# Kernel tuning notes

Hardware: AMD Instinct MI355X
Metric: run time of the kernel (lower is better)

Reference implementation:

```python
import jax, jax.numpy as jnp
import numpy as np
import math

B, N, H = 2, 2048, 256
NUM_HEADS, HEAD_DIM = 8, 32
WIN = 32            # window_size
WIN_LEN = 2 * WIN + 1


def setup_inputs() -> dict:
    key = jax.random.key(0)
    ks = jax.random.split(key, 12)
    s = 0.02
    return {
        "x": jax.random.normal(ks[0], (B, N, 4, H), dtype=jnp.float32),
        "Wq": jax.random.normal(ks[1], (H, H), dtype=jnp.float32) * s,
        "bq": jnp.zeros((H,), jnp.float32),
        "Wk": jax.random.normal(ks[2], (H, H), dtype=jnp.float32) * s,
        "bk": jnp.zeros((H,), jnp.float32),
        "Wv": jax.random.normal(ks[3], (H, H), dtype=jnp.float32) * s,
        "bv": jnp.zeros((H,), jnp.float32),
        "Wo": jax.random.normal(ks[4], (H, 3 * H), dtype=jnp.float32) * s,
        "bo": jnp.zeros((3 * H,), jnp.float32),
        "Wvec": jax.random.normal(ks[5], (H, 2 * H), dtype=jnp.float32) * s,
        "alpha_dot": jnp.float32(1.0),
        "alpha_norm": jnp.float32(1.0),
        "Wg": jax.random.normal(ks[6], (2 * H, H), dtype=jnp.float32) * s,
        "bg": jnp.zeros((H,), jnp.float32),
    }


def reference(x, Wq, bq, Wk, bk, Wv, bv, Wo, bo, Wvec, alpha_dot, alpha_norm, Wg, bg):
    h, d = NUM_HEADS, HEAD_DIM
    scale = 1.0 / math.sqrt(d)

    x_scalar = x[:, :, 0]          # (B,N,H)
    vec = x[:, :, 1:4]             # (B,N,3,H)

    q = (x_scalar @ Wq + bq).reshape(B, N, h, d).transpose(0, 2, 1, 3)  # (B,h,N,d)
    k = (x_scalar @ Wk + bk).reshape(B, N, h, d).transpose(0, 2, 1, 3)
    v = (x_scalar @ Wv + bv).reshape(B, N, h, d).transpose(0, 2, 1, 3)

    vec_proj = vec @ Wvec                                # (B,N,3,2H)
    vec1, vec2 = vec_proj[..., :H], vec_proj[..., H:]
    vec_dot = (vec1 * vec2).sum(axis=-2)                 # (B,N,H)
    vec_norm = jnp.linalg.norm(vec, axis=2)              # (B,N,H)

    # (B,N,3,h,d) -> (B,h,N,3*d)
    vec_flat = vec.reshape(B, N, 3, h, d).transpose(0, 3, 1, 2, 4).reshape(B, h, N, 3 * d)

    # sliding-window attention via padded gather (matches torch unfold semantics)
    BH = B * h
    q_l = q.reshape(BH, N, d)
    k_l = k.reshape(BH, N, d)
    v_l = v.reshape(BH, N, d)
    vec_l = vec_flat.reshape(BH, N, 3 * d)

    pad = ((0, 0), (WIN, WIN), (0, 0))
    k_p = jnp.pad(k_l, pad)
    v_p = jnp.pad(v_l, pad)
    vec_p = jnp.pad(vec_l, pad)

    idx = jnp.arange(N)[:, None] + jnp.arange(WIN_LEN)[None, :]  # (N,WIN_LEN)
    k_win = k_p[:, idx]        # (BH,N,WIN_LEN,d)
    v_win = v_p[:, idx]
    vec_win = vec_p[:, idx]    # (BH,N,WIN_LEN,3d)

    attn_scores = jnp.einsum('bid,biwd->biw', q_l, k_win) * scale
    attn_weights = jax.nn.softmax(attn_scores, axis=-1)  # (BH,N,WIN_LEN)

    x_agg = jnp.einsum('biw,biwd->bid', attn_weights, v_win).reshape(B, h, N, d)
    vec_aggr = jnp.einsum('biw,biwd->bid', attn_weights, vec_win).reshape(B, h, N, 3 * d)

    x_out = x_agg.transpose(0, 2, 1, 3).reshape(B, N, H)
    vec_aggr = vec_aggr.reshape(B, h, N, 3, d).transpose(0, 2, 3, 1, 4).reshape(B, N, 3, H)

    invariants = jnp.concatenate([alpha_dot * vec_dot, alpha_norm * vec_norm], axis=-1)
    gate = jax.nn.sigmoid(invariants @ Wg + bg)[:, :, None, :]   # (B,N,1,H)
    vec_combined = gate * vec_aggr + vec                          # gated add mixing

    o = x_out @ Wo + bo
    o1, o2, o3 = o[..., :H], o[..., H:2 * H], o[..., 2 * H:]
    x_updated = vec_dot * o1 + vec_norm * o2 + o3

    x_final = jnp.concatenate([x_updated[:, :, None], vec_combined], axis=2)  # (B,N,4,H)
    return x_final, attn_weights
```

## Files before the change

### kernel.cpp

```cpp
#include <hip/hip_runtime.h>
#include <math.h>

#define Bc 2
#define Nn 2048
#define Hh 256
#define NH 8
#define Dd 32
#define WIN 32
#define WL 65
#define BN (Bc * Nn)

typedef __attribute__((ext_vector_type(8))) short bf16x8;
typedef __attribute__((ext_vector_type(4))) float f32x4;

__device__ inline short f2bf(float f) {
    union { float f; unsigned u; } v; v.f = f;
    unsigned r = v.u + 0x7fffu + ((v.u >> 16) & 1u);
    return (short)(r >> 16);
}

__global__ __launch_bounds__(256) void castx_kernel(
    const float* __restrict__ x, const float* __restrict__ alpha_norm,
    short* __restrict__ xs_bf, short* __restrict__ vec_bf,
    float* __restrict__ vec_norm, short* __restrict__ inv_bf) {
    const int idx = blockIdx.x * 256 + threadIdx.x;
    const int bn = idx >> 8, ch = idx & 255;
    const size_t base = (size_t)bn * 1024 + ch;
    const float xs = x[base];
    const float v0 = x[base + 256], v1 = x[base + 512], v2 = x[base + 768];
    xs_bf[(size_t)bn * 256 + ch] = f2bf(xs);
    vec_bf[((size_t)0 * BN + bn) * 256 + ch] = f2bf(v0);
    vec_bf[((size_t)1 * BN + bn) * 256 + ch] = f2bf(v1);
    vec_bf[((size_t)2 * BN + bn) * 256 + ch] = f2bf(v2);
    const float nrm = sqrtf(v0 * v0 + v1 * v1 + v2 * v2);
    vec_norm[(size_t)bn * 256 + ch] = nrm;
    inv_bf[(size_t)bn * 512 + 256 + ch] = f2bf(alpha_norm[0] * nrm);
}

__global__ __launch_bounds__(256) void castw_kernel(
    const float* __restrict__ Wq, const float* __restrict__ Wk, const float* __restrict__ Wv,
    const float* __restrict__ Wvec, const float* __restrict__ Wg, const float* __restrict__ Wo,
    short* __restrict__ WqkvT, short* __restrict__ WvecT,
    short* __restrict__ WgT, short* __restrict__ WoT) {
    __shared__ float Ts[32][33];
    const int t = threadIdx.x;
    const int cc = t & 31, r0 = t >> 5;
    const int id = blockIdx.x;
    const float* W; int ldw; short* WT; int ldwt; int n0s, k0, n0d;
    if (id < 192) {
        const int tn = id >> 3, tk = id & 7, sel = tn >> 3;
        W = sel == 0 ? Wq : (sel == 1 ? Wk : Wv); ldw = 256;
        n0s = (tn & 7) * 32; k0 = tk * 32; WT = WqkvT; ldwt = 256; n0d = tn * 32;
    } else if (id < 320) {
        const int id2 = id - 192, tn = id2 >> 3, tk = id2 & 7;
        W = Wvec; ldw = 512; n0s = tn * 32; k0 = tk * 32; WT = WvecT; ldwt = 256; n0d = n0s;
    } else if (id < 448) {
        const int id3 = id - 320, tn = id3 >> 4, tk = id3 & 15;
        W = Wg; ldw = 256; n0s = tn * 32; k0 = tk * 32; WT = WgT; ldwt = 512; n0d = n0s;
    } else {
        const int id4 = id - 448, tn = id4 >> 3, tk = id4 & 7;
        W = Wo; ldw = 768; n0s = tn * 32; k0 = tk * 32; WT = WoT; ldwt = 256; n0d = n0s;
    }
#pragma unroll
    for (int p = 0; p < 4; ++p) {
        const int rr = r0 + p * 8;
        Ts[rr][cc] = W[(size_t)(k0 + rr) * ldw + n0s + cc];
    }
    __syncthreads();
#pragma unroll
    for (int p = 0; p < 4; ++p) {
        const int rr = r0 + p * 8;
        WT[(size_t)(n0d + rr) * ldwt + k0 + cc] = f2bf(Ts[cc][rr]);
    }
}

template<int NT>
__device__ inline void gemm_tiles(const short* __restrict__ A, const short* __restrict__ BT,
                                  int K, int row0, int col0,
                                  short* As, short* Bs, f32x4 acc[2][NT]) {
    const int t = threadIdx.x;
    const int lane = t & 63, wid = t >> 6;
    const int wm = wid & 1, wn = wid >> 1;
    const int quad = lane >> 4, lm = lane & 15;
#pragma unroll
    for (int mt = 0; mt < 2; ++mt)
#pragma unroll
        for (int nt = 0; nt < NT; ++nt) {
            f32x4 z = {0.f, 0.f, 0.f, 0.f};
            acc[mt][nt] = z;
        }
    for (int k0 = 0; k0 < K; k0 += 32) {
        {
            const int row = t >> 2, cg = t & 3;
            *(bf16x8*)&As[row * 40 + cg * 8] =
                *(const bf16x8*)&A[(size_t)(row0 + row) * K + k0 + cg * 8];
        }
#pragma unroll
        for (int p = 0; p < NT / 2; ++p) {
            const int idx = t + p * 256;
            const int col = idx >> 2, cg = idx & 3;
            *(bf16x8*)&Bs[col * 40 + cg * 8] =
                *(const bf16x8*)&BT[(size_t)(col0 + col) * K + k0 + cg * 8];
        }
        __syncthreads();
        bf16x8 af[2], bfr[NT];
#pragma unroll
        for (int mt = 0; mt < 2; ++mt)
            af[mt] = *(bf16x8*)&As[(wm * 32 + mt * 16 + lm) * 40 + quad * 8];
#pragma unroll
        for (int nt = 0; nt < NT; ++nt)
            bfr[nt] = *(bf16x8*)&Bs[(wn * NT * 16 + nt * 16 + lm) * 40 + quad * 8];
#pragma unroll
        for (int mt = 0; mt < 2; ++mt)
#pragma unroll
            for (int nt = 0; nt < NT; ++nt)
                acc[mt][nt] = __builtin_amdgcn_mfma_f32_16x16x32_bf16(
                    af[mt], bfr[nt], acc[mt][nt], 0, 0, 0);
        __syncthreads();
    }
}

__global__ __launch_bounds__(256) void gemm_qkv(
    const short* __restrict__ A, const short* __restrict__ BT,
    const float* __restrict__ bq, const float* __restrict__ bk, const float* __restrict__ bv,
    short* __restrict__ Qb, short* __restrict__ Kb, short* __restrict__ Vb) {
    __shared__ short As[64 * 40];
    __shared__ short Bs[128 * 40];
    f32x4 acc[2][4];
    const int row0 = blockIdx.x * 64, col0 = blockIdx.y * 128;
    gemm_tiles<4>(A, BT, 256, row0, col0, As, Bs, acc);
    const int lane = threadIdx.x & 63, wid = threadIdx.x >> 6;
    const int wm = wid & 1, wn = wid >> 1, quad = lane >> 4, lm = lane & 15;
    const int chunk = col0 >> 8;
    short* dst = chunk == 0 ? Qb : (chunk == 1 ? Kb : Vb);
    const float* bias = chunk == 0 ? bq : (chunk == 1 ? bk : bv);
#pragma unroll
    for (int mt = 0; mt < 2; ++mt)
#pragma unroll
        for (int nt = 0; nt < 4; ++nt) {
            const int col = col0 + wn * 64 + nt * 16 + lm;
            const int cm = col & 255;
            const float bb = bias[cm];
#pragma unroll
            for (int r = 0; r < 4; ++r) {
                const int row = row0 + wm * 32 + mt * 16 + quad * 4 + r;
                dst[(size_t)row * 256 + cm] = f2bf(acc[mt][nt][r] + bb);
            }
        }
}

__global__ __launch_bounds__(256) void gemm_vecdot(
    const short* __restrict__ A, const short* __restrict__ BT,
    const float* __restrict__ alpha_dot,
    float* __restrict__ vec_dot, short* __restrict__ inv_bf) {
    __shared__ short As[3][64 * 40];
    __shared__ short Bs[2][64 * 40];
    const int row0 = blockIdx.x * 64, ch0 = blockIdx.y * 64;
    const int t = threadIdx.x, lane = t & 63, wid = t >> 6;
    const int wm = wid & 1, wn = wid >> 1, quad = lane >> 4, lm = lane & 15;
    f32x4 acc[3][2][2][2];
#pragma unroll
    for (int p = 0; p < 3; ++p)
#pragma unroll
        for (int h = 0; h < 2; ++h)
#pragma unroll
            for (int mt = 0; mt < 2; ++mt)
#pragma unroll
                for (int nt = 0; nt < 2; ++nt) {
                    f32x4 z = {0.f, 0.f, 0.f, 0.f};
                    acc[p][h][mt][nt] = z;
                }
    for (int k0 = 0; k0 < 256; k0 += 32) {
        const int row = t >> 2, cg = t & 3;
#pragma unroll
        for (int p = 0; p < 3; ++p)
            *(bf16x8*)&As[p][row * 40 + cg * 8] =
                *(const bf16x8*)&A[((size_t)p * BN + row0 + row) * 256 + k0 + cg * 8];
#pragma unroll
        for (int h = 0; h < 2; ++h)
            *(bf16x8*)&Bs[h][row * 40 + cg * 8] =
                *(const bf16x8*)&BT[(size_t)(h * 256 + ch0 + row) * 256 + k0 + cg * 8];
        __syncthreads();
        bf16x8 af[3][2], bfr[2][2];
#pragma unroll
        for (int p = 0; p < 3; ++p)
#pragma unroll
            for (int mt = 0; mt < 2; ++mt)
                af[p][mt] = *(bf16x8*)&As[p][(wm * 32 + mt * 16 + lm) * 40 + quad * 8];
#pragma unroll
        for (int h = 0; h < 2; ++h)
#pragma unroll
            for (int nt = 0; nt < 2; ++nt)
                bfr[h][nt] = *(bf16x8*)&Bs[h][(wn * 32 + nt * 16 + lm) * 40 + quad * 8];
#pragma unroll
        for (int p = 0; p < 3; ++p)
#pragma unroll
            for (int h = 0; h < 2; ++h)
#pragma unroll
                for (int mt = 0; mt < 2; ++mt)
#pragma unroll
                    for (int nt = 0; nt < 2; ++nt)
                        acc[p][h][mt][nt] = __builtin_amdgcn_mfma_f32_16x16x32_bf16(
                            af[p][mt], bfr[h][nt], acc[p][h][mt][nt], 0, 0, 0);
        __syncthreads();
    }
    const float ad = alpha_dot[0];
#pragma unroll
    for (int mt = 0; mt < 2; ++mt)
#pragma unroll
        for (int nt = 0; nt < 2; ++nt) {
            const int col = ch0 + wn * 32 + nt * 16 + lm;
#pragma unroll
            for (int r = 0; r < 4; ++r) {
                const int row = row0 + wm * 32 + mt * 16 + quad * 4 + r;
                float dot = 0.f;
#pragma unroll
                for (int p = 0; p < 3; ++p)
                    dot = fmaf(acc[p][0][mt][nt][r], acc[p][1][mt][nt][r], dot);
                vec_dot[(size_t)row * 256 + col] = dot;
                inv_bf[(size_t)row * 512 + col] = f2bf(ad * dot);
            }
        }
}

__global__ __launch_bounds__(256) void gemm_gate(
    const short* __restrict__ A, const short* __restrict__ BT,
    const float* __restrict__ bg, float* __restrict__ gate) {
    __shared__ short As[64 * 40];
    __shared__ short Bs[64 * 40];
    f32x4 acc[2][2];
    const int row0 = blockIdx.x * 64, col0 = blockIdx.y * 64;
    gemm_tiles<2>(A, BT, 512, row0, col0, As, Bs, acc);
    const int lane = threadIdx.x & 63, wid = threadIdx.x >> 6;
    const int wm = wid & 1, wn = wid >> 1, quad = lane >> 4, lm = lane & 15;
#pragma unroll
    for (int mt = 0; mt < 2; ++mt)
#pragma unroll
        for (int nt = 0; nt < 2; ++nt) {
            const int col = col0 + wn * 32 + nt * 16 + lm;
            const float bb = bg[col];
#pragma unroll
            for (int r = 0; r < 4; ++r) {
                const int row = row0 + wm * 32 + mt * 16 + quad * 4 + r;
                const float z = acc[mt][nt][r] + bb;
                gate[(size_t)row * 256 + col] = 1.f / (1.f + __expf(-z));
            }
        }
}

__global__ __launch_bounds__(256) void attn_fused(
    const short* __restrict__ Qb, const short* __restrict__ Kb,
    const short* __restrict__ Vb, const short* __restrict__ vec_bf,
    const float* __restrict__ gate, const float* __restrict__ x,
    float* __restrict__ attnw, float* __restrict__ out, short* __restrict__ xout_bf) {
    const int bh = blockIdx.x >> 6, tile = blockIdx.x & 63;
    const int b = bh >> 3, hd = bh & 7;
    const int i0 = tile * 32;
    const int t = threadIdx.x, lane = t & 63, wid = t >> 6;
    const int wm = wid & 1, wn = wid >> 1, quad = lane >> 4, lm = lane & 15;

    __shared__ __align__(16) short Qs[32 * 40];
    __shared__ __align__(16) short Ks[96 * 40];
    __shared__ __align__(16) float Sc[32 * 100];
    __shared__ __align__(16) short Pb[32 * 104];
    __shared__ __align__(16) short St[128 * 112];

    for (int idx = t; idx < 32 * 104 / 2; idx += 256) ((int*)Pb)[idx] = 0;
    if (t < 128) {
        const int row = t >> 2, cg = t & 3;
        *(bf16x8*)&Qs[row * 40 + cg * 8] =
            *(const bf16x8*)&Qb[((size_t)(b * Nn + i0 + row)) * 256 + hd * 32 + cg * 8];
    }
#pragma unroll
    for (int kk = 0; kk < 2; ++kk) {
        const int idx = t + kk * 256;
        if (idx < 384) {
            const int row = idx >> 2, cg = idx & 3;
            const int j = i0 - WIN + row;
            bf16x8 kv = {0, 0, 0, 0, 0, 0, 0, 0};
            if (j >= 0 && j < Nn)
                kv = *(const bf16x8*)&Kb[((size_t)(b * Nn + j)) * 256 + hd * 32 + cg * 8];
            *(bf16x8*)&Ks[row * 40 + cg * 8] = kv;
        }
    }
    {
        const int chunk = t >> 4, j0 = t & 15;
#pragma unroll
        for (int it = 0; it < 6; ++it) {
            const int jr = j0 + it * 16;
            const int j = i0 - WIN + jr;
            bf16x8 val = {0, 0, 0, 0, 0, 0, 0, 0};
            if (j >= 0 && j < Nn) {
                if (chunk < 4)
                    val = *(const bf16x8*)&Vb[((size_t)(b * Nn + j)) * 256 + hd * 32 + chunk * 8];
                else {
                    const int vc = (chunk - 4) >> 2, d0 = ((chunk - 4) & 3) * 8;
                    val = *(const bf16x8*)&vec_bf[((size_t)vc * BN + b * Nn + j) * 256 + hd * 32 + d0];
                }
            }
#pragma unroll
            for (int u = 0; u < 8; ++u) St[(chunk * 8 + u) * 112 + jr] = val[u];
        }
    }
    __syncthreads();

    {
        const bf16x8 aq = *(bf16x8*)&Qs[(wm * 16 + lm) * 40 + quad * 8];
#pragma unroll
        for (int nt = 0; nt < 3; ++nt) {
            const bf16x8 bk = *(bf16x8*)&Ks[((wn * 3 + nt) * 16 + lm) * 40 + quad * 8];
            f32x4 c = {0.f, 0.f, 0.f, 0.f};
            c = __builtin_amdgcn_mfma_f32_16x16x32_bf16(aq, bk, c, 0, 0, 0);
#pragma unroll
            for (int r = 0; r < 4; ++r)
                Sc[(wm * 16 + quad * 4 + r) * 100 + (wn * 3 + nt) * 16 + lm] = c[r];
        }
    }
    __syncthreads();

    {
        const int i = t >> 3, sub = t & 7;
        float s[9];
#pragma unroll
        for (int k = 0; k < 9; ++k) {
            const int w = sub + 8 * k;
            s[k] = (w <= 64) ? Sc[i * 100 + i + w] * 0.17677669529663687f : -1e30f;
        }
        float m = s[0];
#pragma unroll
        for (int k = 1; k < 9; ++k) m = fmaxf(m, s[k]);
#pragma unroll
        for (int off = 1; off < 8; off <<= 1) m = fmaxf(m, __shfl_xor(m, off, 64));
        float sum = 0.f;
#pragma unroll
        for (int k = 0; k < 9; ++k) {
            const float e = (sub + 8 * k <= 64) ? __expf(s[k] - m) : 0.f;
            s[k] = e;
            sum += e;
        }
#pragma unroll
        for (int off = 1; off < 8; off <<= 1) sum += __shfl_xor(sum, off, 64);
        const float inv = 1.f / sum;
        float* dst = &attnw[((size_t)bh * Nn + (i0 + i)) * WL];
#pragma unroll
        for (int k = 0; k < 9; ++k) {
            const int w = sub + 8 * k;
            if (w <= 64) {
                const float pw = s[k] * inv;
                dst[w] = pw;
                Pb[i * 104 + i + w] = f2bf(pw);
            }
        }
    }
    __syncthreads();

    f32x4 acc[4];
#pragma unroll
    for (int nt = 0; nt < 4; ++nt) {
        f32x4 z = {0.f, 0.f, 0.f, 0.f};
        acc[nt] = z;
    }
#pragma unroll
    for (int ks = 0; ks < 3; ++ks) {
        const bf16x8 ap = *(bf16x8*)&Pb[(wm * 16 + lm) * 104 + ks * 32 + quad * 8];
#pragma unroll
        for (int nt = 0; nt < 4; ++nt) {
            const bf16x8 bs = *(bf16x8*)&St[(wn * 64 + nt * 16 + lm) * 112 + ks * 32 + quad * 8];
            acc[nt] = __builtin_amdgcn_mfma_f32_16x16x32_bf16(ap, bs, acc[nt], 0, 0, 0);
        }
    }
#pragma unroll
    for (int nt = 0; nt < 4; ++nt) {
        const int dim = wn * 64 + nt * 16 + lm;
#pragma unroll
        for (int r = 0; r < 4; ++r) {
            const int i = wm * 16 + quad * 4 + r;
            const size_t bn = (size_t)(b * Nn + i0 + i);
            if (dim < 32) {
                xout_bf[bn * 256 + hd * 32 + dim] = f2bf(acc[nt][r]);
            } else {
                const int dm = dim - 32, c = dm >> 5, dd = dm & 31;
                const int ch = hd * 32 + dd;
                const float g = gate[bn * 256 + ch];
                const size_t off = bn * 1024 + (1 + c) * 256 + ch;
                out[off] = fmaf(g, acc[nt][r], x[off]);
            }
        }
    }
}

__global__ __launch_bounds__(256) void gemm_outf(
    const short* __restrict__ A, const short* __restrict__ BT,
    const float* __restrict__ bo,
    const float* __restrict__ vec_dot, const float* __restrict__ vec_norm,
    float* __restrict__ out) {
    __shared__ short As[64 * 40];
    __shared__ short Bs[3][64 * 40];
    const int row0 = blockIdx.x * 64, ch0 = blockIdx.y * 64;
    const int t = threadIdx.x, lane = t & 63, wid = t >> 6;
    const int wm = wid & 1, wn = wid >> 1, quad = lane >> 4, lm = lane & 15;
    f32x4 acc[3][2][2];
#pragma unroll
    for (int p = 0; p < 3; ++p)
#pragma unroll
        for (int mt = 0; mt < 2; ++mt)
#pragma unroll
            for (int nt = 0; nt < 2; ++nt) {
                f32x4 z = {0.f, 0.f, 0.f, 0.f};
                acc[p][mt][nt] = z;
            }
    for (int k0 = 0; k0 < 256; k0 += 32) {
        const int row = t >> 2, cg = t & 3;
        *(bf16x8*)&As[row * 40 + cg * 8] =
            *(const bf16x8*)&A[(size_t)(row0 + row) * 256 + k0 + cg * 8];
#pragma unroll
        for (int p = 0; p < 3; ++p)
            *(bf16x8*)&Bs[p][row * 40 + cg * 8] =
                *(const bf16x8*)&BT[(size_t)(p * 256 + ch0 + row) * 256 + k0 + cg * 8];
        __syncthreads();
        bf16x8 af[2], bfr[3][2];
#pragma unroll
        for (int mt = 0; mt < 2; ++mt)
            af[mt] = *(bf16x8*)&As[(wm * 32 + mt * 16 + lm) * 40 + quad * 8];
#pragma unroll
        for (int p = 0; p < 3; ++p)
#pragma unroll
            for (int nt = 0; nt < 2; ++nt)
                bfr[p][nt] = *(bf16x8*)&Bs[p][(wn * 32 + nt * 16 + lm) * 40 + quad * 8];
#pragma unroll
        for (int p = 0; p < 3; ++p)
#pragma unroll
            for (int mt = 0; mt < 2; ++mt)
#pragma unroll
                for (int nt = 0; nt < 2; ++nt)
                    acc[p][mt][nt] = __builtin_amdgcn_mfma_f32_16x16x32_bf16(
                        af[mt], bfr[p][nt], acc[p][mt][nt], 0, 0, 0);
        __syncthreads();
    }
#pragma unroll
    for (int mt = 0; mt < 2; ++mt)
#pragma unroll
        for (int nt = 0; nt < 2; ++nt) {
            const int col = ch0 + wn * 32 + nt * 16 + lm;
            const float b1 = bo[col], b2 = bo[256 + col], b3 = bo[512 + col];
#pragma unroll
            for (int r = 0; r < 4; ++r) {
                const int row = row0 + wm * 32 + mt * 16 + quad * 4 + r;
                const float o1 = acc[0][mt][nt][r] + b1;
                const float o2 = acc[1][mt][nt][r] + b2;
                const float o3 = acc[2][mt][nt][r] + b3;
                const float vd = vec_dot[(size_t)row * 256 + col];
                const float vn = vec_norm[(size_t)row * 256 + col];
                out[(size_t)row * 1024 + col] = vd * o1 + vn * o2 + o3;
            }
        }
}

extern "C" void kernel_launch(void* const* d_in, const int* in_sizes, int n_in,
                              void* d_out, int out_size, void* d_ws, size_t ws_size,
                              hipStream_t stream) {
    const float* x  = (const float*)d_in[0];
    const float* Wq = (const float*)d_in[1];
    const float* bq = (const float*)d_in[2];
    const float* Wk = (const float*)d_in[3];
    const float* bk = (const float*)d_in[4];
    const float* Wv = (const float*)d_in[5];
    const float* bv = (const float*)d_in[6];
    const float* Wo = (const float*)d_in[7];
    const float* bo = (const float*)d_in[8];
    const float* Wvec = (const float*)d_in[9];
    const float* alpha_dot  = (const float*)d_in[10];
    const float* alpha_norm = (const float*)d_in[11];
    const float* Wg = (const float*)d_in[12];
    const float* bg = (const float*)d_in[13];

    float* ws = (float*)d_ws;
    float* vec_dot  = ws;
    float* vec_norm = ws + 1048576;
    float* gate     = ws + 2097152;
    short* sb = (short*)(ws + 3145728);
    short* xs_bf   = sb;
    short* vec_bf  = sb + 1048576;
    short* inv_bf  = sb + 4194304;
    short* xout_bf = sb + 6291456;
    short* Q_bf    = sb + 7340032;
    short* K_bf    = sb + 8388608;
    short* V_bf    = sb + 9437184;
    short* WqkvT   = sb + 10485760;
    short* WvecT   = sb + 10682368;
    short* WgT     = sb + 10813440;
    short* WoT     = sb + 10944512;

    float* out = (float*)d_out;
    float* attnw = out + (size_t)Bc * Nn * 4 * Hh;

    castx_kernel<<<4096, 256, 0, stream>>>(x, alpha_norm, xs_bf, vec_bf, vec_norm, inv_bf);
    castw_kernel<<<640, 256, 0, stream>>>(Wq, Wk, Wv, Wvec, Wg, Wo,
                                          WqkvT, WvecT, WgT, WoT);
    gemm_qkv<<<dim3(64, 6), 256, 0, stream>>>(xs_bf, WqkvT, bq, bk, bv, Q_bf, K_bf, V_bf);
    gemm_vecdot<<<dim3(64, 4), 256, 0, stream>>>(vec_bf, WvecT, alpha_dot, vec_dot, inv_bf);
    gemm_gate<<<dim3(64, 4), 256, 0, stream>>>(inv_bf, WgT, bg, gate);
    attn_fused<<<1024, 256, 0, stream>>>(Q_bf, K_bf, V_bf, vec_bf, gate, x,
                                         attnw, out, xout_bf);
    gemm_outf<<<dim3(64, 4), 256, 0, stream>>>(xout_bf, WoT, bo, vec_dot, vec_norm, out);
}
```

Before: 152.8 us.

## Merge cast kernels, register-prefetch GEMM tiles, fuse softmax into QK MFMA wave

Merges the x-cast and weight-transpose kernels into one launch. Adds register prefetch of the next K-slice in the shared GEMM helper, gemm_vecdot and gemm_outf, so global loads overlap with the MFMA work. gemm_vecdot uses 32-column tiles on a doubled grid for more blocks. In the attention kernel the score MFMAs and softmax run in registers on two waves, which removes the Sc shared buffer, one barrier and the St padding. The trade-offs are higher register pressure and two of four waves sitting idle during softmax.

```diff
diff --git a/kernel.cpp b/kernel.cpp
--- a/kernel.cpp
+++ b/kernel.cpp
@@ -19,33 +19,33 @@
     return (short)(r >> 16);
 }
 
-__global__ __launch_bounds__(256) void castx_kernel(
+__global__ __launch_bounds__(256) void castxw_kernel(
     const float* __restrict__ x, const float* __restrict__ alpha_norm,
-    short* __restrict__ xs_bf, short* __restrict__ vec_bf,
-    float* __restrict__ vec_norm, short* __restrict__ inv_bf) {
-    const int idx = blockIdx.x * 256 + threadIdx.x;
-    const int bn = idx >> 8, ch = idx & 255;
-    const size_t base = (size_t)bn * 1024 + ch;
-    const float xs = x[base];
-    const float v0 = x[base + 256], v1 = x[base + 512], v2 = x[base + 768];
-    xs_bf[(size_t)bn * 256 + ch] = f2bf(xs);
-    vec_bf[((size_t)0 * BN + bn) * 256 + ch] = f2bf(v0);
-    vec_bf[((size_t)1 * BN + bn) * 256 + ch] = f2bf(v1);
-    vec_bf[((size_t)2 * BN + bn) * 256 + ch] = f2bf(v2);
-    const float nrm = sqrtf(v0 * v0 + v1 * v1 + v2 * v2);
-    vec_norm[(size_t)bn * 256 + ch] = nrm;
-    inv_bf[(size_t)bn * 512 + 256 + ch] = f2bf(alpha_norm[0] * nrm);
-}
-
-__global__ __launch_bounds__(256) void castw_kernel(
     const float* __restrict__ Wq, const float* __restrict__ Wk, const float* __restrict__ Wv,
     const float* __restrict__ Wvec, const float* __restrict__ Wg, const float* __restrict__ Wo,
+    short* __restrict__ xs_bf, short* __restrict__ vec_bf,
+    float* __restrict__ vec_norm, short* __restrict__ inv_bf,
     short* __restrict__ WqkvT, short* __restrict__ WvecT,
     short* __restrict__ WgT, short* __restrict__ WoT) {
     __shared__ float Ts[32][33];
+    if (blockIdx.x < 4096) {
+        const int idx = blockIdx.x * 256 + threadIdx.x;
+        const int bn = idx >> 8, ch = idx & 255;
+        const size_t base = (size_t)bn * 1024 + ch;
+        const float xs = x[base];
+        const float v0 = x[base + 256], v1 = x[base + 512], v2 = x[base + 768];
+        xs_bf[(size_t)bn * 256 + ch] = f2bf(xs);
+        vec_bf[((size_t)0 * BN + bn) * 256 + ch] = f2bf(v0);
+        vec_bf[((size_t)1 * BN + bn) * 256 + ch] = f2bf(v1);
+        vec_bf[((size_t)2 * BN + bn) * 256 + ch] = f2bf(v2);
+        const float nrm = sqrtf(v0 * v0 + v1 * v1 + v2 * v2);
+        vec_norm[(size_t)bn * 256 + ch] = nrm;
+        inv_bf[(size_t)bn * 512 + 256 + ch] = f2bf(alpha_norm[0] * nrm);
+        return;
+    }
     const int t = threadIdx.x;
     const int cc = t & 31, r0 = t >> 5;
-    const int id = blockIdx.x;
+    const int id = blockIdx.x - 4096;
     const float* W; int ldw; short* WT; int ldwt; int n0s, k0, n0d;
     if (id < 192) {
         const int tn = id >> 3, tk = id & 7, sel = tn >> 3;
@@ -82,6 +82,7 @@
     const int lane = t & 63, wid = t >> 6;
     const int wm = wid & 1, wn = wid >> 1;
     const int quad = lane >> 4, lm = lane & 15;
+    const int srow = t >> 2, scg = (t & 3) * 8;
 #pragma unroll
     for (int mt = 0; mt < 2; ++mt)
 #pragma unroll
@@ -89,20 +90,29 @@
             f32x4 z = {0.f, 0.f, 0.f, 0.f};
             acc[mt][nt] = z;
         }
+    bf16x8 pa = *(const bf16x8*)&A[(size_t)(row0 + srow) * K + scg];
+    bf16x8 pb[NT / 2];
+#pragma unroll
+    for (int p = 0; p < NT / 2; ++p) {
+        const int idx = t + p * 256;
+        pb[p] = *(const bf16x8*)&BT[(size_t)(col0 + (idx >> 2)) * K + (idx & 3) * 8];
+    }
     for (int k0 = 0; k0 < K; k0 += 32) {
-        {
-            const int row = t >> 2, cg = t & 3;
-            *(bf16x8*)&As[row * 40 + cg * 8] =
-                *(const bf16x8*)&A[(size_t)(row0 + row) * K + k0 + cg * 8];
-        }
+        *(bf16x8*)&As[srow * 40 + scg] = pa;
 #pragma unroll
         for (int p = 0; p < NT / 2; ++p) {
             const int idx = t + p * 256;
-            const int col = idx >> 2, cg = idx & 3;
-            *(bf16x8*)&Bs[col * 40 + cg * 8] =
-                *(const bf16x8*)&BT[(size_t)(col0 + col) * K + k0 + cg * 8];
+            *(bf16x8*)&Bs[(idx >> 2) * 40 + (idx & 3) * 8] = pb[p];
         }
         __syncthreads();
+        if (k0 + 32 < K) {
+            pa = *(const bf16x8*)&A[(size_t)(row0 + srow) * K + k0 + 32 + scg];
+#pragma unroll
+            for (int p = 0; p < NT / 2; ++p) {
+                const int idx = t + p * 256;
+                pb[p] = *(const bf16x8*)&BT[(size_t)(col0 + (idx >> 2)) * K + k0 + 32 + (idx & 3) * 8];
+            }
+        }
         bf16x8 af[2], bfr[NT];
 #pragma unroll
         for (int mt = 0; mt < 2; ++mt)
@@ -154,34 +164,40 @@
     const float* __restrict__ alpha_dot,
     float* __restrict__ vec_dot, short* __restrict__ inv_bf) {
     __shared__ short As[3][64 * 40];
-    __shared__ short Bs[2][64 * 40];
-    const int row0 = blockIdx.x * 64, ch0 = blockIdx.y * 64;
+    __shared__ short Bs[2][32 * 40];
+    const int row0 = blockIdx.x * 64, ch0 = blockIdx.y * 32;
     const int t = threadIdx.x, lane = t & 63, wid = t >> 6;
     const int wm = wid & 1, wn = wid >> 1, quad = lane >> 4, lm = lane & 15;
-    f32x4 acc[3][2][2][2];
+    const int srow = t >> 2, scg = (t & 3) * 8;
+    const int bh_ = t >> 7, bc = (t >> 2) & 31, bcg = (t & 3) * 8;
+    f32x4 acc[3][2][2];
 #pragma unroll
     for (int p = 0; p < 3; ++p)
 #pragma unroll
         for (int h = 0; h < 2; ++h)
 #pragma unroll
-            for (int mt = 0; mt < 2; ++mt)
-#pragma unroll
-                for (int nt = 0; nt < 2; ++nt) {
-                    f32x4 z = {0.f, 0.f, 0.f, 0.f};
-                    acc[p][h][mt][nt] = z;
-                }
+            for (int mt = 0; mt < 2; ++mt) {
+                f32x4 z = {0.f, 0.f, 0.f, 0.f};
+                acc[p][h][mt] = z;
+            }
+    bf16x8 pa[3], pb;
+#pragma unroll
+    for (int p = 0; p < 3; ++p)
+        pa[p] = *(const bf16x8*)&A[((size_t)p * BN + row0 + srow) * 256 + scg];
+    pb = *(const bf16x8*)&BT[(size_t)(bh_ * 256 + ch0 + bc) * 256 + bcg];
     for (int k0 = 0; k0 < 256; k0 += 32) {
-        const int row = t >> 2, cg = t & 3;
 #pragma unroll
         for (int p = 0; p < 3; ++p)
-            *(bf16x8*)&As[p][row * 40 + cg * 8] =
-                *(const bf16x8*)&A[((size_t)p * BN + row0 + row) * 256 + k0 + cg * 8];
-#pragma unroll
-        for (int h = 0; h < 2; ++h)
-            *(bf16x8*)&Bs[h][row * 40 + cg * 8] =
-                *(const bf16x8*)&BT[(size_t)(h * 256 + ch0 + row) * 256 + k0 + cg * 8];
+            *(bf16x8*)&As[p][srow * 40 + scg] = pa[p];
+        *(bf16x8*)&Bs[bh_][bc * 40 + bcg] = pb;
         __syncthreads();
-        bf16x8 af[3][2], bfr[2][2];
+        if (k0 + 32 < 256) {
+#pragma unroll
+            for (int p = 0; p < 3; ++p)
+                pa[p] = *(const bf16x8*)&A[((size_t)p * BN + row0 + srow) * 256 + k0 + 32 + scg];
+            pb = *(const bf16x8*)&BT[(size_t)(bh_ * 256 + ch0 + bc) * 256 + k0 + 32 + bcg];
+        }
+        bf16x8 af[3][2], bfr[2];
 #pragma unroll
         for (int p = 0; p < 3; ++p)
 #pragma unroll
@@ -189,38 +205,32 @@
                 af[p][mt] = *(bf16x8*)&As[p][(wm * 32 + mt * 16 + lm) * 40 + quad * 8];
 #pragma unroll
         for (int h = 0; h < 2; ++h)
-#pragma unroll
-            for (int nt = 0; nt < 2; ++nt)
-                bfr[h][nt] = *(bf16x8*)&Bs[h][(wn * 32 + nt * 16 + lm) * 40 + quad * 8];
+            bfr[h] = *(bf16x8*)&Bs[h][(wn * 16 + lm) * 40 + quad * 8];
 #pragma unroll
         for (int p = 0; p < 3; ++p)
 #pragma unroll
             for (int h = 0; h < 2; ++h)
 #pragma unroll
                 for (int mt = 0; mt < 2; ++mt)
-#pragma unroll
-                    for (int nt = 0; nt < 2; ++nt)
-                        acc[p][h][mt][nt] = __builtin_amdgcn_mfma_f32_16x16x32_bf16(
-                            af[p][mt], bfr[h][nt], acc[p][h][mt][nt], 0, 0, 0);
+                    acc[p][h][mt] = __builtin_amdgcn_mfma_f32_16x16x32_bf16(
+                        af[p][mt], bfr[h], acc[p][h][mt], 0, 0, 0);
         __syncthreads();
     }
     const float ad = alpha_dot[0];
 #pragma unroll
-    for (int mt = 0; mt < 2; ++mt)
-#pragma unroll
-        for (int nt = 0; nt < 2; ++nt) {
-            const int col = ch0 + wn * 32 + nt * 16 + lm;
-#pragma unroll
-            for (int r = 0; r < 4; ++r) {
-                const int row = row0 + wm * 32 + mt * 16 + quad * 4 + r;
-                float dot = 0.f;
-#pragma unroll
-                for (int p = 0; p < 3; ++p)
-                    dot = fmaf(acc[p][0][mt][nt][r], acc[p][1][mt][nt][r], dot);
-                vec_dot[(size_t)row * 256 + col] = dot;
-                inv_bf[(size_t)row * 512 + col] = f2bf(ad * dot);
-            }
-        }
+    for (int mt = 0; mt < 2; ++mt) {
+        const int col = ch0 + wn * 16 + lm;
+#pragma unroll
+        for (int r = 0; r < 4; ++r) {
+            const int row = row0 + wm * 32 + mt * 16 + quad * 4 + r;
+            float dot = 0.f;
+#pragma unroll
+            for (int p = 0; p < 3; ++p)
+                dot = fmaf(acc[p][0][mt][r], acc[p][1][mt][r], dot);
+            vec_dot[(size_t)row * 256 + col] = dot;
+            inv_bf[(size_t)row * 512 + col] = f2bf(ad * dot);
+        }
+    }
 }
 
 __global__ __launch_bounds__(256) void gemm_gate(
@@ -261,9 +271,8 @@
 
     __shared__ __align__(16) short Qs[32 * 40];
     __shared__ __align__(16) short Ks[96 * 40];
-    __shared__ __align__(16) float Sc[32 * 100];
     __shared__ __align__(16) short Pb[32 * 104];
-    __shared__ __align__(16) short St[128 * 112];
+    __shared__ __align__(16) short St[128 * 104];
 
     for (int idx = t; idx < 32 * 104 / 2; idx += 256) ((int*)Pb)[idx] = 0;
     if (t < 128) {
@@ -299,58 +308,68 @@
                 }
             }
 #pragma unroll
-            for (int u = 0; u < 8; ++u) St[(chunk * 8 + u) * 112 + jr] = val[u];
+            for (int u = 0; u < 8; ++u) St[(chunk * 8 + u) * 104 + jr] = val[u];
         }
     }
     __syncthreads();
 
-    {
-        const bf16x8 aq = *(bf16x8*)&Qs[(wm * 16 + lm) * 40 + quad * 8];
-#pragma unroll
-        for (int nt = 0; nt < 3; ++nt) {
-            const bf16x8 bk = *(bf16x8*)&Ks[((wn * 3 + nt) * 16 + lm) * 40 + quad * 8];
-            f32x4 c = {0.f, 0.f, 0.f, 0.f};
-            c = __builtin_amdgcn_mfma_f32_16x16x32_bf16(aq, bk, c, 0, 0, 0);
-#pragma unroll
-            for (int r = 0; r < 4; ++r)
-                Sc[(wm * 16 + quad * 4 + r) * 100 + (wn * 3 + nt) * 16 + lm] = c[r];
-        }
-    }
-    __syncthreads();
-
-    {
-        const int i = t >> 3, sub = t & 7;
-        float s[9];
-#pragma unroll
-        for (int k = 0; k < 9; ++k) {
-            const int w = sub + 8 * k;
-            s[k] = (w <= 64) ? Sc[i * 100 + i + w] * 0.17677669529663687f : -1e30f;
-        }
-        float m = s[0];
-#pragma unroll
-        for (int k = 1; k < 9; ++k) m = fmaxf(m, s[k]);
-#pragma unroll
-        for (int off = 1; off < 8; off <<= 1) m = fmaxf(m, __shfl_xor(m, off, 64));
-        float sum = 0.f;
-#pragma unroll
-        for (int k = 0; k < 9; ++k) {
-            const float e = (sub + 8 * k <= 64) ? __expf(s[k] - m) : 0.f;
-            s[k] = e;
-            sum += e;
-        }
-#pragma unroll
-        for (int off = 1; off < 8; off <<= 1) sum += __shfl_xor(sum, off, 64);
-        const float inv = 1.f / sum;
-        float* dst = &attnw[((size_t)bh * Nn + (i0 + i)) * WL];
-#pragma unroll
-        for (int k = 0; k < 9; ++k) {
-            const int w = sub + 8 * k;
-            if (w <= 64) {
-                const float pw = s[k] * inv;
-                dst[w] = pw;
-                Pb[i * 104 + i + w] = f2bf(pw);
-            }
-        }
+    if (wid < 2) {
+        const int il0 = wid * 16;
+        const bf16x8 aq = *(bf16x8*)&Qs[(il0 + lm) * 40 + quad * 8];
+        f32x4 c[6];
+#pragma unroll
+        for (int nt = 0; nt < 6; ++nt) {
+            const bf16x8 bk = *(bf16x8*)&Ks[(nt * 16 + lm) * 40 + quad * 8];
+            f32x4 z = {0.f, 0.f, 0.f, 0.f};
+            c[nt] = __builtin_amdgcn_mfma_f32_16x16x32_bf16(aq, bk, z, 0, 0, 0);
+        }
+        float mx[4] = {-1e30f, -1e30f, -1e30f, -1e30f};
+#pragma unroll
+        for (int nt = 0; nt < 6; ++nt)
+#pragma unroll
+            for (int r = 0; r < 4; ++r) {
+                const int il = il0 + quad * 4 + r;
+                const int w = nt * 16 + lm - il;
+                const float v = (w >= 0 && w <= 64)
+                    ? c[nt][r] * 0.17677669529663687f : -1e30f;
+                c[nt][r] = v;
+                mx[r] = fmaxf(mx[r], v);
+            }
+#pragma unroll
+        for (int off = 1; off < 16; off <<= 1)
+#pragma unroll
+            for (int r = 0; r < 4; ++r) mx[r] = fmaxf(mx[r], __shfl_xor(mx[r], off, 64));
+        float sm[4] = {0.f, 0.f, 0.f, 0.f};
+#pragma unroll
+        for (int nt = 0; nt < 6; ++nt)
+#pragma unroll
+            for (int r = 0; r < 4; ++r) {
+                const int il = il0 + quad * 4 + r;
+                const int w = nt * 16 + lm - il;
+                const float e = (w >= 0 && w <= 64) ? __expf(c[nt][r] - mx[r]) : 0.f;
+                c[nt][r] = e;
+                sm[r] += e;
+            }
+#pragma unroll
+        for (int off = 1; off < 16; off <<= 1)
+#pragma unroll
+            for (int r = 0; r < 4; ++r) sm[r] += __shfl_xor(sm[r], off, 64);
+        float inv[4];
+#pragma unroll
+        for (int r = 0; r < 4; ++r) inv[r] = 1.f / sm[r];
+#pragma unroll
+        for (int nt = 0; nt < 6; ++nt)
+#pragma unroll
+            for (int r = 0; r < 4; ++r) {
+                const int il = il0 + quad * 4 + r;
+                const int jr = nt * 16 + lm;
+                const int w = jr - il;
+                if (w >= 0 && w <= 64) {
+                    const float pw = c[nt][r] * inv[r];
+                    attnw[((size_t)bh * Nn + (i0 + il)) * WL + w] = pw;
+                    Pb[il * 104 + jr] = f2bf(pw);
+                }
+            }
     }
     __syncthreads();
 
@@ -365,7 +384,7 @@
         const bf16x8 ap = *(bf16x8*)&Pb[(wm * 16 + lm) * 104 + ks * 32 + quad * 8];
 #pragma unroll
         for (int nt = 0; nt < 4; ++nt) {
-            const bf16x8 bs = *(bf16x8*)&St[(wn * 64 + nt * 16 + lm) * 112 + ks * 32 + quad * 8];
+            const bf16x8 bs = *(bf16x8*)&St[(wn * 64 + nt * 16 + lm) * 104 + ks * 32 + quad * 8];
             acc[nt] = __builtin_amdgcn_mfma_f32_16x16x32_bf16(ap, bs, acc[nt], 0, 0, 0);
         }
     }
@@ -399,6 +418,7 @@
     const int row0 = blockIdx.x * 64, ch0 = blockIdx.y * 64;
     const int t = threadIdx.x, lane = t & 63, wid = t >> 6;
     const int wm = wid & 1, wn = wid >> 1, quad = lane >> 4, lm = lane & 15;
+    const int srow = t >> 2, scg = (t & 3) * 8;
     f32x4 acc[3][2][2];
 #pragma unroll
     for (int p = 0; p < 3; ++p)
@@ -409,15 +429,23 @@
                 f32x4 z = {0.f, 0.f, 0.f, 0.f};
                 acc[p][mt][nt] = z;
             }
+    bf16x8 pa, pb[3];
+    pa = *(const bf16x8*)&A[(size_t)(row0 + srow) * 256 + scg];
+#pragma unroll
+    for (int p = 0; p < 3; ++p)
+        pb[p] = *(const bf16x8*)&BT[(size_t)(p * 256 + ch0 + srow) * 256 + scg];
     for (int k0 = 0; k0 < 256; k0 += 32) {
-        const int row = t >> 2, cg = t & 3;
-        *(bf16x8*)&As[row * 40 + cg * 8] =
-            *(const bf16x8*)&A[(size_t)(row0 + row) * 256 + k0 + cg * 8];
+        *(bf16x8*)&As[srow * 40 + scg] = pa;
 #pragma unroll
         for (int p = 0; p < 3; ++p)
-            *(bf16x8*)&Bs[p][row * 40 + cg * 8] =
-                *(const bf16x8*)&BT[(size_t)(p * 256 + ch0 + row) * 256 + k0 + cg * 8];
+            *(bf16x8*)&Bs[p][srow * 40 + scg] = pb[p];
         __syncthreads();
+        if (k0 + 32 < 256) {
+            pa = *(const bf16x8*)&A[(size_t)(row0 + srow) * 256 + k0 + 32 + scg];
+#pragma unroll
+            for (int p = 0; p < 3; ++p)
+                pb[p] = *(const bf16x8*)&BT[(size_t)(p * 256 + ch0 + srow) * 256 + k0 + 32 + scg];
+        }
         bf16x8 af[2], bfr[3][2];
 #pragma unroll
         for (int mt = 0; mt < 2; ++mt)
@@ -494,11 +522,11 @@
     float* out = (float*)d_out;
     float* attnw = out + (size_t)Bc * Nn * 4 * Hh;
 
-    castx_kernel<<<4096, 256, 0, stream>>>(x, alpha_norm, xs_bf, vec_bf, vec_norm, inv_bf);
-    castw_kernel<<<640, 256, 0, stream>>>(Wq, Wk, Wv, Wvec, Wg, Wo,
-                                          WqkvT, WvecT, WgT, WoT);
+    castxw_kernel<<<4736, 256, 0, stream>>>(x, alpha_norm, Wq, Wk, Wv, Wvec, Wg, Wo,
+                                            xs_bf, vec_bf, vec_norm, inv_bf,
+                                            WqkvT, WvecT, WgT, WoT);
     gemm_qkv<<<dim3(64, 6), 256, 0, stream>>>(xs_bf, WqkvT, bq, bk, bv, Q_bf, K_bf, V_bf);
-    gemm_vecdot<<<dim3(64, 4), 256, 0, stream>>>(vec_bf, WvecT, alpha_dot, vec_dot, inv_bf);
+    gemm_vecdot<<<dim3(64, 8), 256, 0, stream>>>(vec_bf, WvecT, alpha_dot, vec_dot, inv_bf);
     gemm_gate<<<dim3(64, 4), 256, 0, stream>>>(inv_bf, WgT, bg, gate);
     attn_fused<<<1024, 256, 0, stream>>>(Q_bf, K_bf, V_bf, vec_bf, gate, x,
                                          attnw, out, xout_bf);
```

New measurement: 146.3 us. 4.3% less time.
